# Optimization experiments

Measured on AMD Instinct MI355X. Metric: run time of the kernel, lower is better.

The kernel has to match this reference:

```python
import jax, jax.numpy as jnp
from jax import lax
import numpy as np

BS, J, O, M, E = 256, 50, 50, 50, 64
D = 3 * E  # Set2Set in_channels


def _lstm_cell(x, h, c, Wih, Whh, bih, bhh):
    gates = x @ Wih.T + h @ Whh.T + bih + bhh
    i, f, g, o = jnp.split(gates, 4, axis=-1)
    c = jax.nn.sigmoid(f) * c + jax.nn.sigmoid(i) * jnp.tanh(g)
    h = jax.nn.sigmoid(o) * jnp.tanh(c)
    return h, c


def _lstm_seq(x, Wih, Whh, bih, bhh):
    # x: [B, T, I] -> all hidden states [B, T, H] (torch nn.LSTM, zero init state)
    B = x.shape[0]
    H = Whh.shape[1]
    h0 = jnp.zeros((B, H), x.dtype)

    def step(carry, xt):
        h, c = carry
        h, c = _lstm_cell(xt, h, c, Wih, Whh, bih, bhh)
        return (h, c), h

    _, hs = lax.scan(step, (h0, h0), jnp.swapaxes(x, 0, 1))
    return jnp.swapaxes(hs, 0, 1)


def setup_inputs() -> dict:
    key = jax.random.key(0)
    ks = jax.random.split(key, 24)

    def rn(k, shape, scale=0.05):
        return scale * jax.random.normal(k, shape, dtype=jnp.float32)

    return {
        "job_times": jax.random.uniform(ks[0], (BS, J, O), dtype=jnp.float32),
        # per-(batch,job) permutation of machine ids, as in JSSP
        "precedence": jnp.argsort(jax.random.uniform(ks[1], (BS, J, M)), axis=-1).astype(jnp.int32),
        "job_state": jax.random.randint(ks[2], (BS, J), 0, O + 1, dtype=jnp.int32),
        "job_early_start_time": jax.random.uniform(ks[3], (BS, J), dtype=jnp.float32),
        "machine_utilization": jax.random.uniform(ks[4], (BS, M), dtype=jnp.float32),
        "makespan": jax.random.uniform(ks[5], (BS,), dtype=jnp.float32),
        "Wmac": rn(ks[6], (E, 1)), "bmac": rn(ks[7], (E,)),
        "Wjt": rn(ks[8], (E, 1)), "bjt": rn(ks[9], (E,)),
        "Wih": rn(ks[10], (4 * E, 2 * E)), "Whh": rn(ks[11], (4 * E, E)),
        "bih": rn(ks[12], (4 * E,)), "bhh": rn(ks[13], (4 * E,)),
        "Wdyn": rn(ks[14], (2 * E, 7)), "bdyn": rn(ks[15], (2 * E,)),
        "Wih2": rn(ks[16], (4 * D, 2 * D)), "Whh2": rn(ks[17], (4 * D, D)),
        "bih2": rn(ks[18], (4 * D,)), "bhh2": rn(ks[19], (4 * D,)),
    }


def reference(job_times, precedence, job_state, job_early_start_time,
              machine_utilization, makespan,
              Wmac, bmac, Wjt, bjt, Wih, Whh, bih, bhh,
              Wdyn, bdyn, Wih2, Whh2, bih2, bhh2):
    # ---------- instanceEmbedding ----------
    prec_pad = jnp.concatenate([precedence, jnp.full((BS, J, 1), M, precedence.dtype)], axis=2)  # [BS,J,O+1]
    jt_pad = jnp.concatenate([job_times, jnp.zeros((BS, J, 1), job_times.dtype)], axis=2)        # [BS,J,O+1]
    # Linear(1, E) embeddings applied elementwise
    mac_emb = prec_pad.astype(jnp.float32)[..., None] * Wmac[:, 0] + bmac  # [BS,J,O+1,E]
    jt_emb = jt_pad[..., None] * Wjt[:, 0] + bjt                           # [BS,J,O+1,E]
    pt = jnp.concatenate([mac_emb, jt_emb], axis=-1).reshape(BS * J, O + 1, 2 * E)
    # LSTM over time-reversed op sequences
    job_emb = _lstm_seq(pt[:, ::-1, :], Wih, Whh, bih, bhh).reshape(BS, J, O + 1, E)
    # ---------- dynamicEmbedding ----------
    je = jnp.take_along_axis(job_emb, (O - job_state)[..., None, None], axis=2)[:, :, 0, :]  # [BS,J,E]
    jpt = jnp.take_along_axis(jt_pad, job_state[..., None], axis=2)   # job processing time [BS,J,1]
    jst = job_early_start_time[..., None]                             # [BS,J,1]
    jet = jst + jpt                                                   # job end time
    twr = jnp.cumsum(jt_pad[:, :, ::-1], axis=2)[:, :, ::-1]          # flip-cumsum-flip
    twr = jnp.take_along_axis(twr, job_state[..., None], axis=2)      # total work remaining
    mac_id = jnp.take_along_axis(prec_pad, job_state[..., None], axis=2)[..., 0]  # [BS,J] in [0,M]
    mu_pad = jnp.concatenate([machine_utilization, jnp.zeros((BS, 1), machine_utilization.dtype)], axis=1)
    mu = jnp.take_along_axis(mu_pad, mac_id, axis=1)[..., None]       # [BS,J,1]
    bidx = jnp.arange(BS)[:, None, None]
    jidx = jnp.arange(J)[None, :, None]
    # scatter_: ordered[b,j,precedence[b,j,o]] = job_times[b,j,o]
    ordered = jnp.zeros_like(jt_pad).at[bidx, jidx, precedence].set(job_times)
    twm = ordered.sum(axis=1)                                         # total work per machine [BS,O+1]
    trm = jnp.take_along_axis(twm, mac_id, axis=1)[..., None] - mu    # remaining on machine
    cm = jnp.broadcast_to(makespan[:, None, None], (BS, J, 1))        # current makespan
    feats = jnp.concatenate([jpt, jst, jet, twr, mu, trm, cm], axis=2)  # [BS,J,7]
    dyn = feats @ Wdyn.T + bdyn                                       # [BS,J,2E]
    state = jnp.concatenate([je, dyn], axis=2)                        # [BS,J,3E]
    # ---------- Set2Set(3E, processing_steps=1, num_layers=1) ----------
    q_star = jnp.zeros((BS, 2 * D), state.dtype)
    h = jnp.zeros((BS, D), state.dtype)
    c = h
    for _ in range(1):
        h, c = _lstm_cell(q_star, h, c, Wih2, Whh2, bih2, bhh2)
        e = jnp.einsum('bjd,bd->bj', state, h)
        a = jax.nn.softmax(e, axis=1)
        r = jnp.einsum('bj,bjd->bd', a, state)
        q_star = jnp.concatenate([h, r], axis=1)
    return q_star  # [BS, 2*3E]
```

## Files before the change

### kernel.cpp

```cpp
#include <hip/hip_runtime.h>
#include <hip/hip_bf16.h>
#include <math.h>

#define BS 256
#define J  50
#define O  50
#define MM 50
#define E  64
#define NSEQ (BS*J)
#define G4 (4*E)
#define DD 192
#define NBATCH (NSEQ/32)
#define KH 88

typedef _Float16 f16x8 __attribute__((ext_vector_type(8)));
typedef _Float16 f16x4 __attribute__((ext_vector_type(4)));
typedef _Float16 half2v __attribute__((ext_vector_type(2)));
typedef float f32x16 __attribute__((ext_vector_type(16)));

__device__ float g_u[G4], g_v[G4], g_w[G4];
__device__ float g_h0[E], g_c0[E];
__device__ __align__(16) float g_hc[DD];
__device__ float g_wproj[8];
__device__ float g_cproj;
__device__ float g_je[NSEQ * E];
__device__ int   g_idx[NSEQ];

__device__ __forceinline__ float RCP(float x) {
#if __has_builtin(__builtin_amdgcn_rcpf)
    return __builtin_amdgcn_rcpf(x);
#else
    return __fdividef(1.f, x);
#endif
}
__device__ __forceinline__ float sigm(float x) {
    return RCP(1.f + __expf(-x));
}
__device__ __forceinline__ float ftanh(float x) {
    float e = __expf(-2.f * x);
    return fmaf(2.f, RCP(1.f + e), -1.f);
}

__device__ __forceinline__ half2v PK(float a, float b) {
#if __has_builtin(__builtin_amdgcn_cvt_pkrtz)
    auto t = __builtin_amdgcn_cvt_pkrtz(a, b);
    return __builtin_bit_cast(half2v, t);
#else
    half2v r; r[0] = (_Float16)a; r[1] = (_Float16)b; return r;
#endif
}

__global__ __launch_bounds__(256) void precompute_kernel(
    const float* __restrict__ Wmac, const float* __restrict__ bmac,
    const float* __restrict__ Wjt,  const float* __restrict__ bjt,
    const float* __restrict__ Wih,  const float* __restrict__ bih,
    const float* __restrict__ bhh,
    const float* __restrict__ Wdyn, const float* __restrict__ bdyn,
    const float* __restrict__ bih2, const float* __restrict__ bhh2,
    const int*   __restrict__ job_state)
{
    __shared__ float s_hc[DD];
    __shared__ int cnt51[51], cur51[51];
    const int g = threadIdx.x;

    if (g < 51) cnt51[g] = 0;

    {
        const float* row = &Wih[g * (2 * E)];
        float u = 0.f, v = 0.f, w = 0.f;
        #pragma unroll 8
        for (int e = 0; e < E; ++e) {
            float w0 = row[e], w1 = row[E + e];
            u = fmaf(w0, Wmac[e], u);
            v = fmaf(w1, Wjt[e], v);
            w = fmaf(w0, bmac[e], fmaf(w1, bjt[e], w));
        }
        g_u[g] = u;
        g_v[g] = v;
        g_w[g] = w + bih[g] + bhh[g];
    }

    if (g < DD) {
        float gi = bih2[g]          + bhh2[g];
        float gg = bih2[2 * DD + g] + bhh2[2 * DD + g];
        float go = bih2[3 * DD + g] + bhh2[3 * DD + g];
        float c  = sigm(gi) * ftanh(gg);
        float h  = sigm(go) * ftanh(c);
        s_hc[g] = h;
        g_hc[g] = h;
    }
    __syncthreads();

    if (g < E) {
        float ai = fmaf((float)MM, g_u[g],         g_w[g]);
        float ag = fmaf((float)MM, g_u[2 * E + g], g_w[2 * E + g]);
        float ao = fmaf((float)MM, g_u[3 * E + g], g_w[3 * E + g]);
        float c0 = sigm(ai) * ftanh(ag);
        float h0 = sigm(ao) * ftanh(c0);
        g_h0[g] = h0;
        g_c0[g] = c0;
    }

    if (g < 8) {
        float s = 0.f;
        if (g < 7) {
            for (int d = 0; d < 2 * E; ++d) s = fmaf(s_hc[E + d], Wdyn[d * 7 + g], s);
        }
        g_wproj[g] = s;
    }
    if (g == 8) {
        float s = 0.f;
        for (int d = 0; d < 2 * E; ++d) s = fmaf(s_hc[E + d], bdyn[d], s);
        g_cproj = s;
    }

    for (int s = g; s < NSEQ; s += 256)
        atomicAdd(&cnt51[job_state[s]], 1);
    __syncthreads();
    if (g == 0) {
        int run = 0;
        for (int b2 = 0; b2 < 51; ++b2) { cur51[b2] = run; run += cnt51[b2]; }
    }
    __syncthreads();
    for (int s = g; s < NSEQ; s += 256) {
        int pos = atomicAdd(&cur51[job_state[s]], 1);
        g_idx[pos] = s;
    }
}

__global__ __launch_bounds__(256, 4) void lstm_kernel(
    const float* __restrict__ job_times,
    const int*   __restrict__ precedence,
    const int*   __restrict__ job_state,
    const float* __restrict__ Whh)
{
    __shared__ alignas(16) _Float16 H[2][32 * KH];
    __shared__ half2v Hin[32][O + 1];
    __shared__ int sid_s[32];
    __shared__ int tmx_s[32];
    __shared__ int tmax_sh;

    const int tid  = threadIdx.x;
    const int lane = tid & 63;
    const int wid  = tid >> 6;
    const int n    = lane & 31;
    const int hi   = lane >> 5;
    const int swz  = ((n >> 3) & 3) << 3;

    const int rl = lane & 31;
    f16x8 a[2][5];
    #pragma unroll
    for (int ti = 0; ti < 2; ++ti) {
        const int tile = wid + 4 * ti;
        const int grow = (rl >> 3) * 64 + 8 * tile + (rl & 7);
        const float* wr = Whh + grow * 64 + hi * 8;
        #pragma unroll
        for (int kt = 0; kt < 4; ++kt) {
            f16x8 t;
            #pragma unroll
            for (int j = 0; j < 8; ++j) t[j] = (_Float16)wr[kt * 16 + j];
            a[ti][kt] = t;
        }
        f16x8 t;
        #pragma unroll
        for (int j = 0; j < 8; ++j) t[j] = (_Float16)0.f;
        if (hi == 0) {
            t[0] = (_Float16)g_u[grow];
            t[1] = (_Float16)g_v[grow];
            t[2] = (_Float16)g_w[grow];
        }
        a[ti][4] = t;
    }

    const int ub0 = 8 * wid + 4 * hi;
    const int ub1 = ub0 + 32;
    float h0r[2][4];
    float cr[2][4], hr[2][4];
    #pragma unroll
    for (int x = 0; x < 4; ++x) {
        cr[0][x] = g_c0[ub0 + x]; h0r[0][x] = g_h0[ub0 + x];
        cr[1][x] = g_c0[ub1 + x]; h0r[1][x] = g_h0[ub1 + x];
        hr[0][x] = h0r[0][x];     hr[1][x] = h0r[1][x];
    }

    const int b = blockIdx.x;

    if (tid < 32) {
        int s = g_idx[b * 32 + tid];
        sid_s[tid] = s;
        tmx_s[tid] = O - job_state[s];
    }
    {
        int* Hi = (int*)H;
        for (int i = tid; i < 2 * 32 * KH / 2; i += 256) Hi[i] = 0;
    }
    __syncthreads();
    if (tid == 0) {
        int m = 0;
        for (int i = 0; i < 32; ++i) m = max(m, tmx_s[i]);
        tmax_sh = m;
    }
    for (int i = tid; i < 32 * O; i += 256) {
        const int n2 = i / O;
        const int t2 = i % O + 1;
        const int sid2 = sid_s[n2];
        const int o = O - t2;
        half2v pk = PK((float)precedence[sid2 * MM + o],
                       job_times[sid2 * O + o]);
        Hin[n2][t2] = pk;
        if (t2 == 1) *reinterpret_cast<half2v*>(&H[0][n2 * KH + 64]) = pk;
    }
    {
        f16x4 hv0, hv1;
        #pragma unroll
        for (int x = 0; x < 4; ++x) { hv0[x] = (_Float16)h0r[0][x]; hv1[x] = (_Float16)h0r[1][x]; }
        *reinterpret_cast<f16x4*>(&H[0][n * KH + (ub0 ^ swz)]) = hv0;
        *reinterpret_cast<f16x4*>(&H[0][n * KH + (ub1 ^ swz)]) = hv1;
    }
    if (tid < 32) {
        H[0][tid * KH + 66] = (_Float16)1.f;
        H[1][tid * KH + 66] = (_Float16)1.f;
    }
    __syncthreads();

    const int tmaxM = tmax_sh;
    const int tmaxn = tmx_s[n];
    const int sidn  = sid_s[n];

    int cur = 0;
    for (int t = 1; t <= tmaxM; ++t) {
        const int nxt = cur ^ 1;
        const _Float16* Hc = &H[cur][n * KH];

        f32x16 d0, d1;
        #pragma unroll
        for (int j = 0; j < 16; ++j) { d0[j] = 0.f; d1[j] = 0.f; }
        #pragma unroll
        for (int kt = 0; kt < 5; ++kt) {
            const int kb  = 16 * kt + 8 * hi;
            const int off = (kt < 4) ? (kb ^ swz) : kb;
            f16x8 bf = *reinterpret_cast<const f16x8*>(&Hc[off]);
            d0 = __builtin_amdgcn_mfma_f32_32x32x16_f16(a[0][kt], bf, d0, 0, 0, 0);
            d1 = __builtin_amdgcn_mfma_f32_32x32x16_f16(a[1][kt], bf, d1, 0, 0, 0);
        }

        const bool upd = (t <= tmaxn);
        #pragma unroll
        for (int ti = 0; ti < 2; ++ti) {
            #pragma unroll
            for (int x = 0; x < 4; ++x) {
                const f32x16& d = ti ? d1 : d0;
                float gi = d[x], gf = d[4 + x], gg = d[8 + x], go = d[12 + x];
                float ei = __expf(-gi);
                float ef = __expf(-gf);
                float eg = __expf(-2.f * gg);
                float eo = __expf(-go);
                float sf  = RCP(1.f + ef);
                float itg = (1.f - eg) * RCP((1.f + ei) * (1.f + eg));
                float cn  = fmaf(sf, cr[ti][x], itg);
                float ec  = __expf(-2.f * cn);
                float hn  = (1.f - ec) * RCP((1.f + eo) * (1.f + ec));
                if (upd) { cr[ti][x] = cn; hr[ti][x] = hn; }
            }
        }
        if (upd) {
            f16x4 hv0, hv1;
            #pragma unroll
            for (int x = 0; x < 4; ++x) { hv0[x] = (_Float16)hr[0][x]; hv1[x] = (_Float16)hr[1][x]; }
            *reinterpret_cast<f16x4*>(&H[nxt][n * KH + (ub0 ^ swz)]) = hv0;
            *reinterpret_cast<f16x4*>(&H[nxt][n * KH + (ub1 ^ swz)]) = hv1;
        }
        if (tid < 32 && t < tmaxM) {
            *reinterpret_cast<half2v*>(&H[nxt][tid * KH + 64]) = Hin[tid][t + 1];
        }
        __syncthreads();
        cur = nxt;
    }

    {
        float4 v0 = make_float4(hr[0][0], hr[0][1], hr[0][2], hr[0][3]);
        float4 v1 = make_float4(hr[1][0], hr[1][1], hr[1][2], hr[1][3]);
        *reinterpret_cast<float4*>(&g_je[sidn * E + ub0]) = v0;
        *reinterpret_cast<float4*>(&g_je[sidn * E + ub1]) = v1;
    }
}

__global__ __launch_bounds__(256) void finalize_kernel(
    const float* __restrict__ job_times, const int* __restrict__ precedence,
    const int* __restrict__ job_state,   const float* __restrict__ jest,
    const float* __restrict__ macut,     const float* __restrict__ mksp,
    const float* __restrict__ Wdyn,      const float* __restrict__ bdyn,
    float* __restrict__ out)
{
    const int b   = blockIdx.x;
    const int tid = threadIdx.x;

    __shared__ float rows[J][MM + 2];
    __shared__ float twm[MM + 1];
    __shared__ float feats[J][8];
    __shared__ float aw[J];
    __shared__ float fbar[8];

    for (int i = tid; i < J * (MM + 2); i += 256)
        reinterpret_cast<float*>(rows)[i] = 0.f;
    __syncthreads();

    for (int i = tid; i < J * O; i += 256) {
        const int j = i / O, o = i % O;
        rows[j][precedence[(b * J + j) * MM + o]] = job_times[(b * J + j) * O + o];
    }
    __syncthreads();

    if (tid <= MM) {
        float s = 0.f;
        for (int j = 0; j < J; ++j) s += rows[j][tid];
        twm[tid] = s;
    }
    __syncthreads();

    if (tid < J) {
        const int j  = tid;
        const int js = job_state[b * J + j];
        const float* jt = &job_times[(b * J + j) * O];
        float jpt = (js < O) ? jt[js] : 0.f;
        float jst = jest[b * J + j];
        float twr = 0.f;
        for (int o = js; o < O; ++o) twr += jt[o];
        int   mac = (js < O) ? precedence[(b * J + j) * MM + js] : MM;
        float mu  = (mac < MM) ? macut[b * MM + mac] : 0.f;
        float trm = twm[mac] - mu;
        float cm  = mksp[b];
        float f0 = jpt, f1 = jst, f2 = jst + jpt, f3 = twr, f4 = mu, f5 = trm, f6 = cm;
        feats[j][0] = f0; feats[j][1] = f1; feats[j][2] = f2; feats[j][3] = f3;
        feats[j][4] = f4; feats[j][5] = f5; feats[j][6] = f6; feats[j][7] = 0.f;

        float e = g_cproj;
        e = fmaf(f0, g_wproj[0], e); e = fmaf(f1, g_wproj[1], e);
        e = fmaf(f2, g_wproj[2], e); e = fmaf(f3, g_wproj[3], e);
        e = fmaf(f4, g_wproj[4], e); e = fmaf(f5, g_wproj[5], e);
        e = fmaf(f6, g_wproj[6], e);
        const float4* je4 = reinterpret_cast<const float4*>(&g_je[(b * J + j) * E]);
        const float4* hc4 = reinterpret_cast<const float4*>(g_hc);
        #pragma unroll 4
        for (int d4 = 0; d4 < E / 4; ++d4) {
            float4 jv = je4[d4], hv = hc4[d4];
            e = fmaf(jv.x, hv.x, e); e = fmaf(jv.y, hv.y, e);
            e = fmaf(jv.z, hv.z, e); e = fmaf(jv.w, hv.w, e);
        }
        aw[j] = e;
    }
    __syncthreads();

    if (tid < 64) {
        float v = (tid < J) ? aw[tid] : -1e30f;
        float mx = v;
        #pragma unroll
        for (int off = 32; off >= 1; off >>= 1) mx = fmaxf(mx, __shfl_xor(mx, off));
        float ex = (tid < J) ? __expf(v - mx) : 0.f;
        float sm = ex;
        #pragma unroll
        for (int off = 32; off >= 1; off >>= 1) sm += __shfl_xor(sm, off);
        if (tid < J) aw[tid] = ex * RCP(sm);
    }
    __syncthreads();

    float* ob = out + b * (2 * DD);

    if (tid < 8) {
        float s = 0.f;
        for (int j = 0; j < J; ++j) s = fmaf(aw[j], feats[j][tid], s);
        fbar[tid] = s;
    }
    if (tid < DD) ob[tid] = g_hc[tid];
    if (tid >= 64 && tid < 128) {
        const int d = tid - 64;
        float s = 0.f;
        for (int j = 0; j < J; ++j) s = fmaf(aw[j], g_je[(b * J + j) * E + d], s);
        ob[DD + d] = s;
    }
    __syncthreads();
    if (tid < 2 * E) {
        float s = bdyn[tid];
        const float* wd = &Wdyn[tid * 7];
        #pragma unroll
        for (int f = 0; f < 7; ++f) s = fmaf(fbar[f], wd[f], s);
        ob[DD + E + tid] = s;
    }
}

extern "C" void kernel_launch(void* const* d_in, const int* in_sizes, int n_in,
                              void* d_out, int out_size, void* d_ws, size_t ws_size,
                              hipStream_t stream)
{
    const float* job_times  = (const float*)d_in[0];
    const int*   precedence = (const int*)  d_in[1];
    const int*   job_state  = (const int*)  d_in[2];
    const float* jest       = (const float*)d_in[3];
    const float* macut      = (const float*)d_in[4];
    const float* mksp       = (const float*)d_in[5];
    const float* Wmac       = (const float*)d_in[6];
    const float* bmac       = (const float*)d_in[7];
    const float* Wjt        = (const float*)d_in[8];
    const float* bjt        = (const float*)d_in[9];
    const float* Wih        = (const float*)d_in[10];
    const float* Whh        = (const float*)d_in[11];
    const float* bih        = (const float*)d_in[12];
    const float* bhh        = (const float*)d_in[13];
    const float* Wdyn       = (const float*)d_in[14];
    const float* bdyn       = (const float*)d_in[15];
    const float* bih2       = (const float*)d_in[18];
    const float* bhh2       = (const float*)d_in[19];

    precompute_kernel<<<1, 256, 0, stream>>>(Wmac, bmac, Wjt, bjt, Wih, bih, bhh,
                                             Wdyn, bdyn, bih2, bhh2, job_state);
    lstm_kernel<<<NBATCH, 256, 0, stream>>>(job_times, precedence, job_state, Whh);
    finalize_kernel<<<BS, 256, 0, stream>>>(job_times, precedence, job_state, jest,
                                            macut, mksp, Wdyn, bdyn, (float*)d_out);
}
```

Baseline: 94.53 us.

## Split histogram sort into multi-block kernels and parallelize finalize reductions

The counting sort of sequences by job_state moves out of the single-block precompute kernel into separate multi-block histogram and scatter kernels, with a memset and a device-memory prefix sum. The LSTM kernel drops its LDS XOR swizzle, issues the next-step input write before the MFMAs, and raises wave priority around the MFMA block. The finalize kernel splits the attention dot products and the weighted sum over four thread groups. Each part targets serial work or stalls, at the cost of extra launches and possible LDS bank conflicts without the swizzle.

```diff
diff --git a/kernel.cpp b/kernel.cpp
--- a/kernel.cpp
+++ b/kernel.cpp
@@ -50,6 +50,21 @@
 #endif
 }
 
+__global__ __launch_bounds__(256) void hist_kernel(
+    const int* __restrict__ job_state, int* __restrict__ cnt)
+{
+    const int s = blockIdx.x * 256 + threadIdx.x;
+    atomicAdd(&cnt[job_state[s]], 1);
+}
+
+__global__ __launch_bounds__(256) void scatter_kernel(
+    const int* __restrict__ job_state, int* __restrict__ off)
+{
+    const int s = blockIdx.x * 256 + threadIdx.x;
+    const int pos = atomicAdd(&off[job_state[s]], 1);
+    g_idx[pos] = s;
+}
+
 __global__ __launch_bounds__(256) void precompute_kernel(
     const float* __restrict__ Wmac, const float* __restrict__ bmac,
     const float* __restrict__ Wjt,  const float* __restrict__ bjt,
@@ -57,13 +72,10 @@
     const float* __restrict__ bhh,
     const float* __restrict__ Wdyn, const float* __restrict__ bdyn,
     const float* __restrict__ bih2, const float* __restrict__ bhh2,
-    const int*   __restrict__ job_state)
+    const int* __restrict__ cnt, int* __restrict__ off)
 {
     __shared__ float s_hc[DD];
-    __shared__ int cnt51[51], cur51[51];
     const int g = threadIdx.x;
-
-    if (g < 51) cnt51[g] = 0;
 
     {
         const float* row = &Wih[g * (2 * E)];
@@ -80,6 +92,11 @@
         g_w[g] = w + bih[g] + bhh[g];
     }
 
+    if (g == 0) {
+        int run = 0;
+        for (int b2 = 0; b2 < 51; ++b2) { off[b2] = run; run += cnt[b2]; }
+    }
+
     if (g < DD) {
         float gi = bih2[g]          + bhh2[g];
         float gg = bih2[2 * DD + g] + bhh2[2 * DD + g];
@@ -113,19 +130,6 @@
         for (int d = 0; d < 2 * E; ++d) s = fmaf(s_hc[E + d], bdyn[d], s);
         g_cproj = s;
     }
-
-    for (int s = g; s < NSEQ; s += 256)
-        atomicAdd(&cnt51[job_state[s]], 1);
-    __syncthreads();
-    if (g == 0) {
-        int run = 0;
-        for (int b2 = 0; b2 < 51; ++b2) { cur51[b2] = run; run += cnt51[b2]; }
-    }
-    __syncthreads();
-    for (int s = g; s < NSEQ; s += 256) {
-        int pos = atomicAdd(&cur51[job_state[s]], 1);
-        g_idx[pos] = s;
-    }
 }
 
 __global__ __launch_bounds__(256, 4) void lstm_kernel(
@@ -145,7 +149,6 @@
     const int wid  = tid >> 6;
     const int n    = lane & 31;
     const int hi   = lane >> 5;
-    const int swz  = ((n >> 3) & 3) << 3;
 
     const int rl = lane & 31;
     f16x8 a[2][5];
@@ -214,8 +217,8 @@
         f16x4 hv0, hv1;
         #pragma unroll
         for (int x = 0; x < 4; ++x) { hv0[x] = (_Float16)h0r[0][x]; hv1[x] = (_Float16)h0r[1][x]; }
-        *reinterpret_cast<f16x4*>(&H[0][n * KH + (ub0 ^ swz)]) = hv0;
-        *reinterpret_cast<f16x4*>(&H[0][n * KH + (ub1 ^ swz)]) = hv1;
+        *reinterpret_cast<f16x4*>(&H[0][n * KH + ub0]) = hv0;
+        *reinterpret_cast<f16x4*>(&H[0][n * KH + ub1]) = hv1;
     }
     if (tid < 32) {
         H[0][tid * KH + 66] = (_Float16)1.f;
@@ -232,17 +235,22 @@
         const int nxt = cur ^ 1;
         const _Float16* Hc = &H[cur][n * KH];
 
+        if (tid < 32 && t < tmaxM) {
+            *reinterpret_cast<half2v*>(&H[nxt][tid * KH + 64]) = Hin[tid][t + 1];
+        }
+
+        __builtin_amdgcn_s_setprio(1);
         f32x16 d0, d1;
         #pragma unroll
         for (int j = 0; j < 16; ++j) { d0[j] = 0.f; d1[j] = 0.f; }
         #pragma unroll
         for (int kt = 0; kt < 5; ++kt) {
-            const int kb  = 16 * kt + 8 * hi;
-            const int off = (kt < 4) ? (kb ^ swz) : kb;
-            f16x8 bf = *reinterpret_cast<const f16x8*>(&Hc[off]);
+            const int kb = 16 * kt + 8 * hi;
+            f16x8 bf = *reinterpret_cast<const f16x8*>(&Hc[kb]);
             d0 = __builtin_amdgcn_mfma_f32_32x32x16_f16(a[0][kt], bf, d0, 0, 0, 0);
             d1 = __builtin_amdgcn_mfma_f32_32x32x16_f16(a[1][kt], bf, d1, 0, 0, 0);
         }
+        __builtin_amdgcn_s_setprio(0);
 
         const bool upd = (t <= tmaxn);
         #pragma unroll
@@ -267,11 +275,8 @@
             f16x4 hv0, hv1;
             #pragma unroll
             for (int x = 0; x < 4; ++x) { hv0[x] = (_Float16)hr[0][x]; hv1[x] = (_Float16)hr[1][x]; }
-            *reinterpret_cast<f16x4*>(&H[nxt][n * KH + (ub0 ^ swz)]) = hv0;
-            *reinterpret_cast<f16x4*>(&H[nxt][n * KH + (ub1 ^ swz)]) = hv1;
-        }
-        if (tid < 32 && t < tmaxM) {
-            *reinterpret_cast<half2v*>(&H[nxt][tid * KH + 64]) = Hin[tid][t + 1];
+            *reinterpret_cast<f16x4*>(&H[nxt][n * KH + ub0]) = hv0;
+            *reinterpret_cast<f16x4*>(&H[nxt][n * KH + ub1]) = hv1;
         }
         __syncthreads();
         cur = nxt;
@@ -299,6 +304,8 @@
     __shared__ float twm[MM + 1];
     __shared__ float feats[J][8];
     __shared__ float aw[J];
+    __shared__ float paw[J][4];
+    __shared__ float pmix[4][64];
     __shared__ float fbar[8];
 
     for (int i = tid; i < J * (MM + 2); i += 256)
@@ -308,6 +315,19 @@
     for (int i = tid; i < J * O; i += 256) {
         const int j = i / O, o = i % O;
         rows[j][precedence[(b * J + j) * MM + o]] = job_times[(b * J + j) * O + o];
+    }
+    if (tid < 4 * J) {
+        const int j = tid >> 2, q = tid & 3;
+        const float4* je4 = reinterpret_cast<const float4*>(&g_je[(b * J + j) * E]);
+        const float4* hc4 = reinterpret_cast<const float4*>(g_hc);
+        float s = 0.f;
+        #pragma unroll
+        for (int d4 = 4 * q; d4 < 4 * q + 4; ++d4) {
+            float4 jv = je4[d4], hv = hc4[d4];
+            s = fmaf(jv.x, hv.x, s); s = fmaf(jv.y, hv.y, s);
+            s = fmaf(jv.z, hv.z, s); s = fmaf(jv.w, hv.w, s);
+        }
+        paw[j][q] = s;
     }
     __syncthreads();
 
@@ -339,15 +359,7 @@
         e = fmaf(f2, g_wproj[2], e); e = fmaf(f3, g_wproj[3], e);
         e = fmaf(f4, g_wproj[4], e); e = fmaf(f5, g_wproj[5], e);
         e = fmaf(f6, g_wproj[6], e);
-        const float4* je4 = reinterpret_cast<const float4*>(&g_je[(b * J + j) * E]);
-        const float4* hc4 = reinterpret_cast<const float4*>(g_hc);
-        #pragma unroll 4
-        for (int d4 = 0; d4 < E / 4; ++d4) {
-            float4 jv = je4[d4], hv = hc4[d4];
-            e = fmaf(jv.x, hv.x, e); e = fmaf(jv.y, hv.y, e);
-            e = fmaf(jv.z, hv.z, e); e = fmaf(jv.w, hv.w, e);
-        }
-        aw[j] = e;
+        aw[j] = e + paw[j][0] + paw[j][1] + paw[j][2] + paw[j][3];
     }
     __syncthreads();
 
@@ -366,25 +378,31 @@
 
     float* ob = out + b * (2 * DD);
 
+    {
+        const int q = tid >> 6, d = tid & 63;
+        const int j0 = (q * J) / 4, j1 = ((q + 1) * J) / 4;
+        float s = 0.f;
+        for (int j = j0; j < j1; ++j)
+            s = fmaf(aw[j], g_je[(b * J + j) * E + d], s);
+        pmix[q][d] = s;
+    }
     if (tid < 8) {
         float s = 0.f;
         for (int j = 0; j < J; ++j) s = fmaf(aw[j], feats[j][tid], s);
         fbar[tid] = s;
     }
     if (tid < DD) ob[tid] = g_hc[tid];
-    if (tid >= 64 && tid < 128) {
-        const int d = tid - 64;
-        float s = 0.f;
-        for (int j = 0; j < J; ++j) s = fmaf(aw[j], g_je[(b * J + j) * E + d], s);
-        ob[DD + d] = s;
-    }
-    __syncthreads();
-    if (tid < 2 * E) {
-        float s = bdyn[tid];
-        const float* wd = &Wdyn[tid * 7];
+    __syncthreads();
+    if (tid < 64) {
+        ob[DD + tid] = pmix[0][tid] + pmix[1][tid] + pmix[2][tid] + pmix[3][tid];
+    }
+    if (tid >= 64 && tid < 192) {
+        const int g = tid - 64;
+        float s = bdyn[g];
+        const float* wd = &Wdyn[g * 7];
         #pragma unroll
         for (int f = 0; f < 7; ++f) s = fmaf(fbar[f], wd[f], s);
-        ob[DD + E + tid] = s;
+        ob[DD + E + g] = s;
     }
 }
 
@@ -411,8 +429,14 @@
     const float* bih2       = (const float*)d_in[18];
     const float* bhh2       = (const float*)d_in[19];
 
+    int* cnt = (int*)d_ws;
+    int* off = cnt + 64;
+
+    hipMemsetAsync(d_ws, 0, 128 * sizeof(int), stream);
+    hist_kernel<<<50, 256, 0, stream>>>(job_state, cnt);
     precompute_kernel<<<1, 256, 0, stream>>>(Wmac, bmac, Wjt, bjt, Wih, bih, bhh,
-                                             Wdyn, bdyn, bih2, bhh2, job_state);
+                                             Wdyn, bdyn, bih2, bhh2, cnt, off);
+    scatter_kernel<<<50, 256, 0, stream>>>(job_state, off);
     lstm_kernel<<<NBATCH, 256, 0, stream>>>(job_times, precedence, job_state, Whh);
     finalize_kernel<<<BS, 256, 0, stream>>>(job_times, precedence, job_state, jest,
                                             macut, mksp, Wdyn, bdyn, (float*)d_out);
```

New measurement: 130.0 us. +37.5%, slower.
